# Optimization experiments

Hardware: AMD Instinct MI355X
Metric: run time of the kernel (lower is better)

Reference implementation:

```python
import jax, jax.numpy as jnp
import numpy as np

B, L, H, P, A, T = 64, 256, 1024, 64, 512, 8


def setup_inputs() -> dict:
    key = jax.random.key(0)
    ks = jax.random.split(key, 9)
    return {
        "word_hiddens": jax.random.normal(ks[0], (B, L, H), dtype=jnp.float32),
        "pos_e1_embeddings": jax.random.normal(ks[1], (B, L, P), dtype=jnp.float32),
        "pos_e2_embeddings": jax.random.normal(ks[2], (B, L, P), dtype=jnp.float32),
        "e1_end": jax.random.randint(ks[3], (B,), 0, L, dtype=jnp.int32),
        "e2_end": jax.random.randint(ks[4], (B,), 0, L, dtype=jnp.int32),
        "type_embeddings": jax.random.normal(ks[5], (T, H), dtype=jnp.float32) * 0.03,
        "W_pos": jax.random.normal(ks[6], (H + 2 * P, A), dtype=jnp.float32) * 0.03,
        "W_ent": jax.random.normal(ks[7], (4 * H, A), dtype=jnp.float32) * 0.02,
        "v": jax.random.normal(ks[8], (A,), dtype=jnp.float32) * 0.05,
    }


def _latent_type(e_h, type_emb):
    # alpha = softmax(e_h @ C^T); latent type = alpha @ C   (C: [T, latent])
    scores = jnp.einsum("bh,th->bt", e_h, type_emb)
    alpha = jax.nn.softmax(scores, axis=-1)
    return jnp.einsum("bt,th->bh", alpha, type_emb)


def reference(word_hiddens, pos_e1_embeddings, pos_e2_embeddings, e1_end, e2_end,
              type_embeddings, W_pos, W_ent, v):
    b, seq_len, h = word_hiddens.shape
    batch_idx = jnp.arange(b)
    e1_h = word_hiddens[batch_idx, e1_end]          # [B, H]
    e2_h = word_hiddens[batch_idx, e2_end]          # [B, H]
    e1_type = _latent_type(e1_h, type_embeddings)   # [B, H]
    e2_type = _latent_type(e2_h, type_embeddings)   # [B, H]

    entity_features = jnp.concatenate([e1_h, e1_type, e2_h, e2_type], axis=-1)  # [B, 4H]
    pos_features = jnp.concatenate([word_hiddens, pos_e1_embeddings, pos_e2_embeddings], axis=-1)  # [B, L, H+2P]

    dense_pos = jnp.einsum("blf,fa->bla", pos_features, W_pos)   # [B, L, A]
    dense_ent = entity_features @ W_ent                          # [B, A]
    # Faithful to original tf.repeat(axis=1)+reshape (element-interleaved, not a broadcast)
    dense_ent_r = jnp.repeat(dense_ent, seq_len, axis=1).reshape(b, seq_len, -1)  # [B, L, A]

    u = jnp.tanh(dense_pos + dense_ent_r)            # [B, L, A]
    vu = jnp.einsum("bla,a->bl", u, v)               # [B, L]
    alpha = jax.nn.softmax(vu, axis=-1)              # [B, L]
    z = jnp.einsum("blh,bl->bh", word_hiddens, alpha)  # [B, H]
    return z
```

## Files before the change

kernel.cpp:

```cpp
#include <hip/hip_runtime.h>
#include <hip/hip_bf16.h>
#include <math.h>

#define B_ 64
#define L_ 256
#define H_ 1024
#define P_ 64
#define A_ 512
#define T_ 8
#define NSTEP 36

typedef __attribute__((ext_vector_type(8))) __bf16 bf16x8;
typedef __attribute__((ext_vector_type(4))) float f32x4;

__device__ __forceinline__ float bf2f(ushort u) {
  union { unsigned int i; float f; } v; v.i = ((unsigned int)u) << 16; return v.f;
}
__device__ __forceinline__ ushort f2bf_rne(float f) {
  union { float f; unsigned int i; } v; v.f = f;
  unsigned int r = v.i + 0x7FFFu + ((v.i >> 16) & 1u);
  return (ushort)(r >> 16);
}
__device__ __forceinline__ unsigned int pack2_rne(float a, float b) {
  return (unsigned int)f2bf_rne(a) | ((unsigned int)f2bf_rne(b) << 16);
}

template <bool BF16>
__device__ __forceinline__ float ld1(const void* p, size_t i) {
  if (BF16) return bf2f(((const ushort*)p)[i]);
  return ((const float*)p)[i];
}
template <bool BF16>
__device__ __forceinline__ float4 ld4(const void* p, size_t i) {
  if (BF16) {
    ushort4 u = *(const ushort4*)((const ushort*)p + i);
    return (float4){bf2f(u.x), bf2f(u.y), bf2f(u.z), bf2f(u.w)};
  }
  return *(const float4*)((const float*)p + i);
}

template <bool BF16>
__global__ __launch_bounds__(256) void prep_k(
    const void* __restrict__ wpos, ushort* __restrict__ WTs,
    const void* __restrict__ wh, const int* __restrict__ e1e,
    const int* __restrict__ e2e, const void* __restrict__ temb,
    float* __restrict__ EF) {
  if (blockIdx.x < 576) {
    __shared__ ushort tile[32][33];
    const int s  = blockIdx.x >> 4;
    const int at = blockIdx.x & 15;
    const int tx = threadIdx.x & 31;
    const int ty = threadIdx.x >> 5;
#pragma unroll
    for (int i = 0; i < 4; ++i) {
      size_t idx = (size_t)(s * 32 + ty + i * 8) * A_ + at * 32 + tx;
      ushort u;
      if (BF16) u = ((const ushort*)wpos)[idx];
      else u = f2bf_rne(((const float*)wpos)[idx]);
      tile[ty + i * 8][tx] = u;
    }
    __syncthreads();
#pragma unroll
    for (int i = 0; i < 4; ++i) {
      WTs[(size_t)s * (A_ * 32) + (size_t)(at * 32 + ty + i * 8) * 32 + tx] =
          tile[tx][ty + i * 8];
    }
  } else {
    const int b = blockIdx.x - 576;
    const int tid = threadIdx.x;
    __shared__ float eh1[1024];
    __shared__ float eh2[1024];
    __shared__ float part[256][16];
    __shared__ float scores[16];
    __shared__ float alpha[16];

    const size_t o1 = ((size_t)b * L_ + e1e[b]) * H_;
    const size_t o2 = ((size_t)b * L_ + e2e[b]) * H_;
    for (int h = tid; h < 1024; h += 256) {
      eh1[h] = ld1<BF16>(wh, o1 + h);
      eh2[h] = ld1<BF16>(wh, o2 + h);
    }
    __syncthreads();

    float p[16];
#pragma unroll
    for (int t = 0; t < 16; ++t) p[t] = 0.f;
    for (int h = tid; h < 1024; h += 256) {
      float a1 = eh1[h], a2 = eh2[h];
#pragma unroll
      for (int t = 0; t < 8; ++t) {
        float c = ld1<BF16>(temb, t * 1024 + h);
        p[t] += a1 * c;
        p[8 + t] += a2 * c;
      }
    }
#pragma unroll
    for (int t = 0; t < 16; ++t) part[tid][t] = p[t];
    __syncthreads();
    if (tid < 16) {
      float s = 0.f;
      for (int i = 0; i < 256; ++i) s += part[i][tid];
      scores[tid] = s;
    }
    __syncthreads();
    if (tid < 2) {
      const int base = tid * 8;
      float mx = scores[base];
      for (int t = 1; t < 8; ++t) mx = fmaxf(mx, scores[base + t]);
      float sum = 0.f;
      float e[8];
      for (int t = 0; t < 8; ++t) { e[t] = __expf(scores[base + t] - mx); sum += e[t]; }
      float inv = 1.f / sum;
      for (int t = 0; t < 8; ++t) alpha[base + t] = e[t] * inv;
    }
    __syncthreads();

    float* efb = EF + (size_t)b * 4096;
    for (int h = tid; h < 1024; h += 256) {
      float l1 = 0.f, l2 = 0.f;
#pragma unroll
      for (int t = 0; t < 8; ++t) {
        float c = ld1<BF16>(temb, t * 1024 + h);
        l1 += alpha[t] * c;
        l2 += alpha[8 + t] * c;
      }
      efb[h] = eh1[h];
      efb[1024 + h] = l1;
      efb[2048 + h] = eh2[h];
      efb[3072 + h] = l2;
    }
  }
}

template <bool BF16>
__global__ __launch_bounds__(256) void ent_gemm(const float* __restrict__ EF,
                                                const void* __restrict__ went,
                                                float* __restrict__ part) {
  const int mh = blockIdx.x & 1;
  const int nb = (blockIdx.x >> 1) & 3;
  const int kb = blockIdx.x >> 3;
  const int tid = threadIdx.x;
  __shared__ float efs[32][128];

  const int k0 = kb * 128;
  {
    const int kq = (tid & 31) * 4;
    for (int m = tid >> 5; m < 32; m += 8) {
      *(float4*)&efs[m][kq] = *(const float4*)&EF[(size_t)(mh * 32 + m) * 4096 + k0 + kq];
    }
  }
  __syncthreads();

  const int n0 = nb * 128 + (tid & 31) * 4;
  const int mg = (tid >> 5) * 4;
  float acc[4][4];
#pragma unroll
  for (int i = 0; i < 4; ++i)
#pragma unroll
    for (int j = 0; j < 4; ++j) acc[i][j] = 0.f;

#pragma unroll 4
  for (int k = 0; k < 128; ++k) {
    float4 w = ld4<BF16>(went, (size_t)(k0 + k) * A_ + n0);
#pragma unroll
    for (int i = 0; i < 4; ++i) {
      float e = efs[mg + i][k];
      acc[i][0] += e * w.x;
      acc[i][1] += e * w.y;
      acc[i][2] += e * w.z;
      acc[i][3] += e * w.w;
    }
  }
#pragma unroll
  for (int i = 0; i < 4; ++i) {
    *(float4*)&part[((size_t)kb * 64 + mh * 32 + mg + i) * A_ + n0] =
        (float4){acc[i][0], acc[i][1], acc[i][2], acc[i][3]};
  }
}

__global__ __launch_bounds__(256) void ent_reduce(const float* __restrict__ part,
                                                  float* __restrict__ dense_ent) {
  const int idx = blockIdx.x * 256 + threadIdx.x;
  float s = 0.f;
#pragma unroll
  for (int kb = 0; kb < 32; ++kb) s += part[(size_t)kb * 32768 + idx];
  dense_ent[idx] = s;
}

template <bool BF16>
__global__ __launch_bounds__(256, 2) void fused_gemm_vu(
    const void* __restrict__ wh, const void* __restrict__ pe1,
    const void* __restrict__ pe2, const ushort* __restrict__ WTs,
    const float* __restrict__ dense_ent, const void* __restrict__ vvec,
    float* __restrict__ vu_part) {
  __shared__ __align__(16) ushort Abuf[2][128 * 32];
  __shared__ __align__(16) ushort Bbuf[2][128 * 32];
  __shared__ float vu_s[4][128];

  const int tid = threadIdx.x;
  const int pid = blockIdx.x;
  const int wid = (pid & 7) * 64 + (pid >> 3);
  const int nb = wid & 3;
  const int mb = wid >> 2;
  const int rbase = mb * 128;
  const int wave = tid >> 6;
  const int lane = tid & 63;
  const int quad = lane >> 4;
  const int col = lane & 15;
  const int wr = wave >> 1;
  const int wc = wave & 1;

  int aoff[4], boff[4];
#pragma unroll
  for (int mf = 0; mf < 4; ++mf) {
    const int ra = wr * 64 + mf * 16 + col;
    aoff[mf] = ra * 32 + ((quad ^ ((ra >> 1) & 3)) << 3);
    const int rb = wc * 64 + mf * 16 + col;
    boff[mf] = rb * 32 + ((quad ^ ((rb >> 1) & 3)) << 3);
  }

  const int brow = tid >> 1;
  const int bc0 = (tid & 1) * 2;
  const int sB0 = brow * 32 + ((bc0 ^ ((brow >> 1) & 3)) << 3);
  const size_t bsrc_off = (size_t)(nb * 128 + brow) * 32 + (size_t)(tid & 1) * 16;

  const int ar0 = tid >> 2, aq = tid & 3;
  const int ar1 = 64 + ar0;
  const int sA0 = ar0 * 32 + ((aq ^ ((ar0 >> 1) & 3)) << 3);
  const int sA1 = ar1 * 32 + ((aq ^ ((ar1 >> 1) & 3)) << 3);

  f32x4 acc[4][4];
#pragma unroll
  for (int i = 0; i < 4; ++i)
#pragma unroll
    for (int j = 0; j < 4; ++j) acc[i][j] = (f32x4){0.f, 0.f, 0.f, 0.f};

  float4 fX0a, fX0b, fX1a, fX1b; uint4 uX0, uX1; uint4 bX0, bX1;
  float4 fY0a, fY0b, fY1a, fY1b; uint4 uY0, uY1; uint4 bY0, bY1;

  auto ISSUE_X = [&](int s) {
    const void* src; int ld, k0;
    if (s < 32)      { src = wh;  ld = H_; k0 = s * 32; }
    else if (s < 34) { src = pe1; ld = P_; k0 = (s - 32) * 32; }
    else             { src = pe2; ld = P_; k0 = (s - 34) * 32; }
    if (BF16) {
      const ushort* p = (const ushort*)src + (size_t)(rbase + brow) * ld + k0 + (tid & 1) * 16;
      uX0 = *(const uint4*)p;
      uX1 = *(const uint4*)(p + 8);
    } else {
      const float* p0 = (const float*)src + (size_t)(rbase + ar0) * ld + k0 + aq * 8;
      fX0a = *(const float4*)p0;
      fX0b = *(const float4*)(p0 + 4);
      const float* p1 = (const float*)src + (size_t)(rbase + ar1) * ld + k0 + aq * 8;
      fX1a = *(const float4*)p1;
      fX1b = *(const float4*)(p1 + 4);
    }
    const ushort* bs = WTs + (size_t)s * (A_ * 32) + bsrc_off;
    bX0 = *(const uint4*)bs;
    bX1 = *(const uint4*)(bs + 8);
  };
  auto ISSUE_Y = [&](int s) {
    const void* src; int ld, k0;
    if (s < 32)      { src = wh;  ld = H_; k0 = s * 32; }
    else if (s < 34) { src = pe1; ld = P_; k0 = (s - 32) * 32; }
    else             { src = pe2; ld = P_; k0 = (s - 34) * 32; }
    if (BF16) {
      const ushort* p = (const ushort*)src + (size_t)(rbase + brow) * ld + k0 + (tid & 1) * 16;
      uY0 = *(const uint4*)p;
      uY1 = *(const uint4*)(p + 8);
    } else {
      const float* p0 = (const float*)src + (size_t)(rbase + ar0) * ld + k0 + aq * 8;
      fY0a = *(const float4*)p0;
      fY0b = *(const float4*)(p0 + 4);
      const float* p1 = (const float*)src + (size_t)(rbase + ar1) * ld + k0 + aq * 8;
      fY1a = *(const float4*)p1;
      fY1b = *(const float4*)(p1 + 4);
    }
    const ushort* bs = WTs + (size_t)s * (A_ * 32) + bsrc_off;
    bY0 = *(const uint4*)bs;
    bY1 = *(const uint4*)(bs + 8);
  };
  auto STORE_X = [&](int buf) {
    if (BF16) {
      *(uint4*)&Abuf[buf][sB0] = uX0;
      *(uint4*)&Abuf[buf][sB0 ^ 8] = uX1;
    } else {
      uint4 u0 = {pack2_rne(fX0a.x, fX0a.y), pack2_rne(fX0a.z, fX0a.w),
                  pack2_rne(fX0b.x, fX0b.y), pack2_rne(fX0b.z, fX0b.w)};
      *(uint4*)&Abuf[buf][sA0] = u0;
      uint4 u1 = {pack2_rne(fX1a.x, fX1a.y), pack2_rne(fX1a.z, fX1a.w),
                  pack2_rne(fX1b.x, fX1b.y), pack2_rne(fX1b.z, fX1b.w)};
      *(uint4*)&Abuf[buf][sA1] = u1;
    }
    *(uint4*)&Bbuf[buf][sB0] = bX0;
    *(uint4*)&Bbuf[buf][sB0 ^ 8] = bX1;
  };
  auto STORE_Y = [&](int buf) {
    if (BF16) {
      *(uint4*)&Abuf[buf][sB0] = uY0;
      *(uint4*)&Abuf[buf][sB0 ^ 8] = uY1;
    } else {
      uint4 u0 = {pack2_rne(fY0a.x, fY0a.y), pack2_rne(fY0a.z, fY0a.w),
                  pack2_rne(fY0b.x, fY0b.y), pack2_rne(fY0b.z, fY0b.w)};
      *(uint4*)&Abuf[buf][sA0] = u0;
      uint4 u1 = {pack2_rne(fY1a.x, fY1a.y), pack2_rne(fY1a.z, fY1a.w),
                  pack2_rne(fY1b.x, fY1b.y), pack2_rne(fY1b.z, fY1b.w)};
      *(uint4*)&Abuf[buf][sA1] = u1;
    }
    *(uint4*)&Bbuf[buf][sB0] = bY0;
    *(uint4*)&Bbuf[buf][sB0 ^ 8] = bY1;
  };
  auto COMPUTE = [&](int buf) {
    bf16x8 af[4], bfr[4];
#pragma unroll
    for (int mf = 0; mf < 4; ++mf) af[mf] = *(const bf16x8*)&Abuf[buf][aoff[mf]];
#pragma unroll
    for (int nf = 0; nf < 4; ++nf) bfr[nf] = *(const bf16x8*)&Bbuf[buf][boff[nf]];
#pragma unroll
    for (int mf = 0; mf < 4; ++mf)
#pragma unroll
      for (int nf = 0; nf < 4; ++nf)
        acc[mf][nf] =
            __builtin_amdgcn_mfma_f32_16x16x32_bf16(af[mf], bfr[nf], acc[mf][nf], 0, 0, 0);
  };

  ISSUE_X(0);
  ISSUE_Y(1);
  STORE_X(0);
  __syncthreads();

  for (int s = 0; s < NSTEP; s += 2) {
    if (s + 2 < NSTEP) ISSUE_X(s + 2);
    COMPUTE(0);
    STORE_Y(1);
    __syncthreads();
    if (s + 3 < NSTEP) ISSUE_Y(s + 3);
    COMPUTE(1);
    if (s + 2 < NSTEP) {
      STORE_X(0);
      __syncthreads();
    }
  }

  float vv[4];
#pragma unroll
  for (int nf = 0; nf < 4; ++nf)
    vv[nf] = ld1<BF16>(vvec, nb * 128 + wc * 64 + nf * 16 + col);

#pragma unroll
  for (int mf = 0; mf < 4; ++mf) {
    const int row0 = wr * 64 + mf * 16 + quad * 4;
    const int r0 = rbase + row0;
    const int bidx = r0 >> 8;
    const int l0 = r0 & 255;
    const float* ebase = dense_ent + bidx * A_ + 2 * l0 + (nb >> 1);
    float e0 = ebase[0], e1 = ebase[2], e2 = ebase[4], e3 = ebase[6];
    float s0 = 0.f, s1 = 0.f, s2 = 0.f, s3 = 0.f;
#pragma unroll
    for (int nf = 0; nf < 4; ++nf) {
      float vn = vv[nf];
      s0 += tanhf(acc[mf][nf][0] + e0) * vn;
      s1 += tanhf(acc[mf][nf][1] + e1) * vn;
      s2 += tanhf(acc[mf][nf][2] + e2) * vn;
      s3 += tanhf(acc[mf][nf][3] + e3) * vn;
    }
    s0 += __shfl_xor(s0, 1); s0 += __shfl_xor(s0, 2); s0 += __shfl_xor(s0, 4); s0 += __shfl_xor(s0, 8);
    s1 += __shfl_xor(s1, 1); s1 += __shfl_xor(s1, 2); s1 += __shfl_xor(s1, 4); s1 += __shfl_xor(s1, 8);
    s2 += __shfl_xor(s2, 1); s2 += __shfl_xor(s2, 2); s2 += __shfl_xor(s2, 4); s2 += __shfl_xor(s2, 8);
    s3 += __shfl_xor(s3, 1); s3 += __shfl_xor(s3, 2); s3 += __shfl_xor(s3, 4); s3 += __shfl_xor(s3, 8);
    if (col == 0) {
      vu_s[wave][row0 + 0] = s0;
      vu_s[wave][row0 + 1] = s1;
      vu_s[wave][row0 + 2] = s2;
      vu_s[wave][row0 + 3] = s3;
    }
  }
  __syncthreads();
  if (tid < 128) {
    const int wrr = tid >> 6;
    float s = vu_s[wrr * 2][tid] + vu_s[wrr * 2 + 1][tid];
    vu_part[(size_t)nb * (B_ * L_) + rbase + tid] = s;
  }
}

template <bool BF16>
__global__ __launch_bounds__(256) void softmax_z(const void* __restrict__ wh,
                                                 const float* __restrict__ vu_part,
                                                 void* __restrict__ out) {
  const int b = blockIdx.x >> 2;
  const int hq = blockIdx.x & 3;
  const int tid = threadIdx.x;
  __shared__ float alpha[256];
  __shared__ float red[256];

  float x = 0.f;
#pragma unroll
  for (int p = 0; p < 4; ++p) x += vu_part[(size_t)p * (B_ * L_) + b * L_ + tid];
  red[tid] = x;
  __syncthreads();
  for (int s = 128; s > 0; s >>= 1) {
    if (tid < s) red[tid] = fmaxf(red[tid], red[tid + s]);
    __syncthreads();
  }
  float m = red[0];
  __syncthreads();
  float e = __expf(x - m);
  red[tid] = e;
  __syncthreads();
  for (int s = 128; s > 0; s >>= 1) {
    if (tid < s) red[tid] += red[tid + s];
    __syncthreads();
  }
  alpha[tid] = e / red[0];
  __syncthreads();

  const int h = hq * 256 + tid;
  const size_t base = (size_t)b * L_ * H_ + h;
  float a0 = 0.f, a1 = 0.f, a2 = 0.f, a3 = 0.f;
  float a4 = 0.f, a5 = 0.f, a6 = 0.f, a7 = 0.f;
  for (int l = 0; l < 256; l += 8) {
    a0 += alpha[l + 0] * ld1<BF16>(wh, base + (size_t)(l + 0) * H_);
    a1 += alpha[l + 1] * ld1<BF16>(wh, base + (size_t)(l + 1) * H_);
    a2 += alpha[l + 2] * ld1<BF16>(wh, base + (size_t)(l + 2) * H_);
    a3 += alpha[l + 3] * ld1<BF16>(wh, base + (size_t)(l + 3) * H_);
    a4 += alpha[l + 4] * ld1<BF16>(wh, base + (size_t)(l + 4) * H_);
    a5 += alpha[l + 5] * ld1<BF16>(wh, base + (size_t)(l + 5) * H_);
    a6 += alpha[l + 6] * ld1<BF16>(wh, base + (size_t)(l + 6) * H_);
    a7 += alpha[l + 7] * ld1<BF16>(wh, base + (size_t)(l + 7) * H_);
  }
  float z = ((a0 + a1) + (a2 + a3)) + ((a4 + a5) + (a6 + a7));
  if (BF16) ((ushort*)out)[b * H_ + h] = f2bf_rne(z);
  else ((float*)out)[b * H_ + h] = z;
}

extern "C" void kernel_launch(void* const* d_in, const int* in_sizes, int n_in,
                              void* d_out, int out_size, void* d_ws, size_t ws_size,
                              hipStream_t stream) {
  const void* wh   = d_in[0];
  const void* pe1  = d_in[1];
  const void* pe2  = d_in[2];
  const int*  e1e  = (const int*)d_in[3];
  const int*  e2e  = (const int*)d_in[4];
  const void* temb = d_in[5];
  const void* wpos = d_in[6];
  const void* went = d_in[7];
  const void* vvec = d_in[8];

  const bool bf16 = (in_sizes[0] == (int)(B_ * L_ * H_ * 2));

  char* ws = (char*)d_ws;
  ushort* WTs      = (ushort*)ws;
  float* dense_ent = (float*)(ws + 1179648);
  float* vu_part   = (float*)(ws + 1310720);
  float* EF        = (float*)(ws + 1310720);
  float* part      = (float*)(ws + 2359296);

  if (bf16) {
    prep_k<true ><<<dim3(640), dim3(256), 0, stream>>>(wpos, WTs, wh, e1e, e2e, temb, EF);
    ent_gemm<true ><<<dim3(256), dim3(256), 0, stream>>>(EF, went, part);
    ent_reduce<<<dim3(128), dim3(256), 0, stream>>>(part, dense_ent);
    fused_gemm_vu<true ><<<dim3(512), dim3(256), 0, stream>>>(wh, pe1, pe2, WTs, dense_ent, vvec, vu_part);
    softmax_z<true ><<<dim3(256), dim3(256), 0, stream>>>(wh, vu_part, d_out);
  } else {
    prep_k<false><<<dim3(640), dim3(256), 0, stream>>>(wpos, WTs, wh, e1e, e2e, temb, EF);
    ent_gemm<false><<<dim3(256), dim3(256), 0, stream>>>(EF, went, part);
    ent_reduce<<<dim3(128), dim3(256), 0, stream>>>(part, dense_ent);
    fused_gemm_vu<false><<<dim3(512), dim3(256), 0, stream>>>(wh, pe1, pe2, WTs, dense_ent, vvec, vu_part);
    softmax_z<false><<<dim3(256), dim3(256), 0, stream>>>(wh, vu_part, d_out);
  }
}
```

Before: 193.3 us.

## Deepen GEMM pipeline to four LDS stages with register prefetch and MFMA priority

Measured after the change: 223.3 us. 15.5% more time.

```diff
diff --git a/kernel.cpp b/kernel.cpp
--- a/kernel.cpp
+++ b/kernel.cpp
@@ -159,7 +159,6 @@
 #pragma unroll
     for (int j = 0; j < 4; ++j) acc[i][j] = 0.f;
 
-#pragma unroll 4
   for (int k = 0; k < 128; ++k) {
     float4 w = ld4<BF16>(went, (size_t)(k0 + k) * A_ + n0);
 #pragma unroll
@@ -193,8 +192,8 @@
     const void* __restrict__ pe2, const ushort* __restrict__ WTs,
     const float* __restrict__ dense_ent, const void* __restrict__ vvec,
     float* __restrict__ vu_part) {
-  __shared__ __align__(16) ushort Abuf[2][128 * 32];
-  __shared__ __align__(16) ushort Bbuf[2][128 * 32];
+  __shared__ __align__(16) ushort Abuf[4][128 * 32];
+  __shared__ __align__(16) ushort Bbuf[4][128 * 32];
   __shared__ float vu_s[4][128];
 
   const int tid = threadIdx.x;
@@ -235,111 +234,84 @@
 #pragma unroll
     for (int j = 0; j < 4; ++j) acc[i][j] = (f32x4){0.f, 0.f, 0.f, 0.f};
 
-  float4 fX0a, fX0b, fX1a, fX1b; uint4 uX0, uX1; uint4 bX0, bX1;
-  float4 fY0a, fY0b, fY1a, fY1b; uint4 uY0, uY1; uint4 bY0, bY1;
-
-  auto ISSUE_X = [&](int s) {
+  struct Set {
+    float4 f0a, f0b, f1a, f1b;
+    uint4 u0, u1;
+    uint4 b0, b1;
+  };
+  Set sx, sy, sz, sw;
+
+  auto issue = [&](Set& S, int s) {
     const void* src; int ld, k0;
     if (s < 32)      { src = wh;  ld = H_; k0 = s * 32; }
     else if (s < 34) { src = pe1; ld = P_; k0 = (s - 32) * 32; }
     else             { src = pe2; ld = P_; k0 = (s - 34) * 32; }
     if (BF16) {
       const ushort* p = (const ushort*)src + (size_t)(rbase + brow) * ld + k0 + (tid & 1) * 16;
-      uX0 = *(const uint4*)p;
-      uX1 = *(const uint4*)(p + 8);
+      S.u0 = *(const uint4*)p;
+      S.u1 = *(const uint4*)(p + 8);
     } else {
       const float* p0 = (const float*)src + (size_t)(rbase + ar0) * ld + k0 + aq * 8;
-      fX0a = *(const float4*)p0;
-      fX0b = *(const float4*)(p0 + 4);
+      S.f0a = *(const float4*)p0;
+      S.f0b = *(const float4*)(p0 + 4);
       const float* p1 = (const float*)src + (size_t)(rbase + ar1) * ld + k0 + aq * 8;
-      fX1a = *(const float4*)p1;
-      fX1b = *(const float4*)(p1 + 4);
+      S.f1a = *(const float4*)p1;
+      S.f1b = *(const float4*)(p1 + 4);
     }
     const ushort* bs = WTs + (size_t)s * (A_ * 32) + bsrc_off;
-    bX0 = *(const uint4*)bs;
-    bX1 = *(const uint4*)(bs + 8);
+    S.b0 = *(const uint4*)bs;
+    S.b1 = *(const uint4*)(bs + 8);
   };
-  auto ISSUE_Y = [&](int s) {
-    const void* src; int ld, k0;
-    if (s < 32)      { src = wh;  ld = H_; k0 = s * 32; }
-    else if (s < 34) { src = pe1; ld = P_; k0 = (s - 32) * 32; }
-    else             { src = pe2; ld = P_; k0 = (s - 34) * 32; }
+  auto store = [&](const Set& S, int buf) {
     if (BF16) {
-      const ushort* p = (const ushort*)src + (size_t)(rbase + brow) * ld + k0 + (tid & 1) * 16;
-      uY0 = *(const uint4*)p;
-      uY1 = *(const uint4*)(p + 8);
+      *(uint4*)&Abuf[buf][sB0] = S.u0;
+      *(uint4*)&Abuf[buf][sB0 ^ 8] = S.u1;
     } else {
-      const float* p0 = (const float*)src + (size_t)(rbase + ar0) * ld + k0 + aq * 8;
-      fY0a = *(const float4*)p0;
-      fY0b = *(const float4*)(p0 + 4);
-      const float* p1 = (const float*)src + (size_t)(rbase + ar1) * ld + k0 + aq * 8;
-      fY1a = *(const float4*)p1;
-      fY1b = *(const float4*)(p1 + 4);
-    }
-    const ushort* bs = WTs + (size_t)s * (A_ * 32) + bsrc_off;
-    bY0 = *(const uint4*)bs;
-    bY1 = *(const uint4*)(bs + 8);
+      uint4 u0 = {pack2_rne(S.f0a.x, S.f0a.y), pack2_rne(S.f0a.z, S.f0a.w),
+                  pack2_rne(S.f0b.x, S.f0b.y), pack2_rne(S.f0b.z, S.f0b.w)};
+      *(uint4*)&Abuf[buf][sA0] = u0;
+      uint4 u1 = {pack2_rne(S.f1a.x, S.f1a.y), pack2_rne(S.f1a.z, S.f1a.w),
+                  pack2_rne(S.f1b.x, S.f1b.y), pack2_rne(S.f1b.z, S.f1b.w)};
+      *(uint4*)&Abuf[buf][sA1] = u1;
+    }
+    *(uint4*)&Bbuf[buf][sB0] = S.b0;
+    *(uint4*)&Bbuf[buf][sB0 ^ 8] = S.b1;
   };
-  auto STORE_X = [&](int buf) {
-    if (BF16) {
-      *(uint4*)&Abuf[buf][sB0] = uX0;
-      *(uint4*)&Abuf[buf][sB0 ^ 8] = uX1;
-    } else {
-      uint4 u0 = {pack2_rne(fX0a.x, fX0a.y), pack2_rne(fX0a.z, fX0a.w),
-                  pack2_rne(fX0b.x, fX0b.y), pack2_rne(fX0b.z, fX0b.w)};
-      *(uint4*)&Abuf[buf][sA0] = u0;
-      uint4 u1 = {pack2_rne(fX1a.x, fX1a.y), pack2_rne(fX1a.z, fX1a.w),
-                  pack2_rne(fX1b.x, fX1b.y), pack2_rne(fX1b.z, fX1b.w)};
-      *(uint4*)&Abuf[buf][sA1] = u1;
-    }
-    *(uint4*)&Bbuf[buf][sB0] = bX0;
-    *(uint4*)&Bbuf[buf][sB0 ^ 8] = bX1;
-  };
-  auto STORE_Y = [&](int buf) {
-    if (BF16) {
-      *(uint4*)&Abuf[buf][sB0] = uY0;
-      *(uint4*)&Abuf[buf][sB0 ^ 8] = uY1;
-    } else {
-      uint4 u0 = {pack2_rne(fY0a.x, fY0a.y), pack2_rne(fY0a.z, fY0a.w),
-                  pack2_rne(fY0b.x, fY0b.y), pack2_rne(fY0b.z, fY0b.w)};
-      *(uint4*)&Abuf[buf][sA0] = u0;
-      uint4 u1 = {pack2_rne(fY1a.x, fY1a.y), pack2_rne(fY1a.z, fY1a.w),
-                  pack2_rne(fY1b.x, fY1b.y), pack2_rne(fY1b.z, fY1b.w)};
-      *(uint4*)&Abuf[buf][sA1] = u1;
-    }
-    *(uint4*)&Bbuf[buf][sB0] = bY0;
-    *(uint4*)&Bbuf[buf][sB0 ^ 8] = bY1;
-  };
-  auto COMPUTE = [&](int buf) {
+  auto compute = [&](int buf) {
     bf16x8 af[4], bfr[4];
 #pragma unroll
     for (int mf = 0; mf < 4; ++mf) af[mf] = *(const bf16x8*)&Abuf[buf][aoff[mf]];
 #pragma unroll
     for (int nf = 0; nf < 4; ++nf) bfr[nf] = *(const bf16x8*)&Bbuf[buf][boff[nf]];
+    __builtin_amdgcn_s_setprio(1);
 #pragma unroll
     for (int mf = 0; mf < 4; ++mf)
 #pragma unroll
       for (int nf = 0; nf < 4; ++nf)
         acc[mf][nf] =
             __builtin_amdgcn_mfma_f32_16x16x32_bf16(af[mf], bfr[nf], acc[mf][nf], 0, 0, 0);
+    __builtin_amdgcn_s_setprio(0);
   };
 
-  ISSUE_X(0);
-  ISSUE_Y(1);
-  STORE_X(0);
-  __syncthreads();
-
-  for (int s = 0; s < NSTEP; s += 2) {
-    if (s + 2 < NSTEP) ISSUE_X(s + 2);
-    COMPUTE(0);
-    STORE_Y(1);
-    __syncthreads();
-    if (s + 3 < NSTEP) ISSUE_Y(s + 3);
-    COMPUTE(1);
-    if (s + 2 < NSTEP) {
-      STORE_X(0);
-      __syncthreads();
-    }
+  issue(sx, 0); issue(sy, 1); issue(sz, 2); issue(sw, 3);
+  store(sx, 0); store(sy, 1);
+  __syncthreads();
+
+  for (int s = 0; s < NSTEP; s += 4) {
+    if (s + 4 < NSTEP) issue(sx, s + 4);
+    compute(0);
+    store(sz, 2);
+    if (s + 5 < NSTEP) issue(sy, s + 5);
+    compute(1);
+    store(sw, 3);
+    __syncthreads();
+    if (s + 6 < NSTEP) issue(sz, s + 6);
+    compute(2);
+    if (s + 4 < NSTEP) store(sx, 0);
+    if (s + 7 < NSTEP) issue(sw, s + 7);
+    compute(3);
+    if (s + 5 < NSTEP) store(sy, 1);
+    __syncthreads();
   }
 
   float vv[4];
```
